# Kernel tuning notes

Measured on AMD Instinct MI355X. Metric: run time of the kernel, lower is better.

The kernel has to match this reference:

```python
import jax, jax.numpy as jnp
import numpy as np
from jax import lax


def setup_inputs() -> dict:
    key = jax.random.key(0)
    ks = jax.random.split(key, 5)
    B, Cin, H, W = 16, 64, 64, 64
    HID, K = 128, 3
    x = jax.random.normal(ks[0], (B, Cin, H, W), jnp.float32)
    w_is = jax.random.normal(ks[1], (4 * HID, Cin, 1, K), jnp.float32) * 0.05
    b_is = jax.random.normal(ks[2], (4 * HID,), jnp.float32) * 0.05
    w_ss = jax.random.normal(ks[3], (4 * HID, HID, 1, K), jnp.float32) * 0.05
    b_ss = jax.random.normal(ks[4], (4 * HID,), jnp.float32) * 0.05
    return {"x": x, "w_is": w_is, "b_is": b_is, "w_ss": w_ss, "b_ss": b_ss}


def reference(x, w_is, b_is, w_ss, b_ss):
    # Shapes: x [B,Cin,H,W]; w_is [4h,Cin,1,k]; w_ss [4h,h,1,k]
    hid = w_ss.shape[1]
    k = w_is.shape[-1]
    pad = k // 2

    # MaskedConv2d mask type 'B' on a (1,k) kernel: keep center and left taps,
    # zero everything strictly right of center.
    mask = (jnp.arange(k) <= pad).astype(x.dtype)  # [k]
    w_is_m = w_is * mask[None, None, None, :]

    # Input-to-state conv over the whole image at once: [B,4h,H,W]
    z_is = lax.conv_general_dilated(
        x, w_is_m, window_strides=(1, 1), padding=[(0, 0), (pad, pad)]
    ) + b_is[None, :, None, None]

    # State-to-state conv is a 1D conv along W: kernel [4h, h, k]
    w1 = w_ss[:, :, 0, :]

    def step(carry, z_row):
        h, c = carry  # each [B, hid, W]
        z = z_row + lax.conv_general_dilated(
            h, w1, window_strides=(1,), padding=[(pad, pad)],
            dimension_numbers=("NCH", "OIH", "NCH"),
        ) + b_ss[None, :, None]
        i_g = jax.nn.sigmoid(z[:, :hid])
        f_g = jax.nn.sigmoid(z[:, hid:2 * hid])
        o_g = jax.nn.sigmoid(z[:, 2 * hid:3 * hid])
        g = jnp.tanh(z[:, 3 * hid:])
        c = f_g * c + i_g * g
        h = o_g * jnp.tanh(c)
        return (h, c), h

    B, _, H, W = x.shape
    h0 = jnp.zeros((B, hid, W), x.dtype)
    c0 = jnp.zeros((B, hid, W), x.dtype)
    zs = jnp.transpose(z_is, (2, 0, 1, 3))  # [H, B, 4h, W]
    _, hs = lax.scan(step, (h0, c0), zs)    # hs: [H, B, hid, W]
    return jnp.transpose(hs, (1, 2, 0, 3))  # [B, hid, H, W]
```

## Files before the change

### kernel.cpp

```cpp
#include <hip/hip_runtime.h>
#include <hip/hip_bf16.h>

#define B_    16
#define CIN   64
#define Hn    64
#define Wn    64
#define HID   128
#define SXS2  72
#define SHS   136
#define NJC   8
#define NBLK  (B_ * NJC)

typedef __attribute__((ext_vector_type(8))) short bfrag_t;
typedef __attribute__((ext_vector_type(4))) float f4_t;

#define HBUF_SHORTS (B_ * Wn * HID)
#define HBUF_BYTES  (HBUF_SHORTS * 2)
#define FLG_STRIDE  256

static __device__ __forceinline__ short f2bf(float f) {
    union { __hip_bfloat16 h; short s; } u;
    u.h = __float2bfloat16(f);
    return u.s;
}
static __device__ __forceinline__ float sigm(float z)  { return 1.f / (1.f + __expf(-z)); }
static __device__ __forceinline__ float tanhf_(float z){ return 2.f / (1.f + __expf(-2.f * z)) - 1.f; }

#define BAR_LGKM() do { \
    asm volatile("s_waitcnt lgkmcnt(0)" ::: "memory"); \
    __builtin_amdgcn_s_barrier(); \
    __builtin_amdgcn_sched_barrier(0); \
} while (0)

#define BAR_VM() do { \
    asm volatile("s_waitcnt vmcnt(0)" ::: "memory"); \
    __builtin_amdgcn_s_barrier(); \
    __builtin_amdgcn_sched_barrier(0); \
} while (0)

extern "C" __global__ __launch_bounds__(256, 1)
void rowlstm_kernel(const float* __restrict__ x,
                    const float* __restrict__ w_is,
                    const float* __restrict__ b_is,
                    const float* __restrict__ w_ss,
                    const float* __restrict__ b_ss,
                    float* __restrict__ out,
                    unsigned char* __restrict__ ws)
{
    const int tid  = threadIdx.x;
    const int bid  = blockIdx.x;
    const int b    = bid & 15;
    const int jc   = bid >> 4;
    const int lane = tid & 63;
    const int wv   = tid >> 6;
    const int l15  = lane & 15;
    const int quad = lane >> 4;

    short*    hbuf0 = (short*)ws;
    unsigned* flags = (unsigned*)(ws + 2 * HBUF_BYTES + b * FLG_STRIDE);

    __shared__ alignas(16) short sH[66 * SHS];
    __shared__ alignas(16) short sX2[65 * SXS2];

    bfrag_t a_frag[4][16];
    #pragma unroll
    for (int mt = 0; mt < 4; ++mt) {
        const int co = mt * HID + jc * 16 + l15;
        #pragma unroll
        for (int kt = 0; kt < 16; ++kt) {
            const int kk0 = kt * 32 + quad * 8;
            const float* p;
            if      (kt < 2)  p = &w_is[(co * CIN + kk0)         * 3 + 0];
            else if (kt < 4)  p = &w_is[(co * CIN + (kk0 - 64))  * 3 + 1];
            else if (kt < 8)  p = &w_ss[(co * HID + (kk0 - 128)) * 3 + 0];
            else if (kt < 12) p = &w_ss[(co * HID + (kk0 - 256)) * 3 + 1];
            else              p = &w_ss[(co * HID + (kk0 - 384)) * 3 + 2];
            bfrag_t v;
            #pragma unroll
            for (int j = 0; j < 8; ++j) v[j] = f2bf(p[j * 3]);
            a_frag[mt][kt] = v;
        }
    }

    float bias[4][4];
    #pragma unroll
    for (int g = 0; g < 4; ++g) {
        #pragma unroll
        for (int r = 0; r < 4; ++r) {
            const int co = g * HID + jc * 16 + quad * 4 + r;
            bias[g][r] = b_is[co] + b_ss[co];
        }
    }

    {
        bfrag_t z8 = {0,0,0,0,0,0,0,0};
        if (tid < 8)  *(bfrag_t*)&sX2[tid * 8] = z8;
        if (tid < 16) {
            *(bfrag_t*)&sH[tid * 8] = z8;
            *(bfrag_t*)&sH[65 * SHS + tid * 8] = z8;
        }
    }

    float creg[4] = {0.f, 0.f, 0.f, 0.f};
    const int wp  = wv * 16 + l15;

    const int xw  = tid & 63;
    const int xc2 = tid >> 6;
    float xr[16];
    #pragma unroll
    for (int e = 0; e < 16; ++e)
        xr[e] = x[((b * CIN + xc2 * 16 + e) * Hn + 0) * Wn + xw];

    const int cig = tid & 15;
    const int w0  = tid >> 4;

    __syncthreads();

    for (int h = 0; h < Hn; ++h) {
        const short* rd_hb = hbuf0 + ((h & 1) ^ 1) * HBUF_SHORTS + b * Wn * HID;
        short*       wr_hb = hbuf0 + (h & 1) * HBUF_SHORTS + b * Wn * HID;

        if (h > 0 && wv == 0) {
            const unsigned tgt = (unsigned)h;
            for (;;) {
                unsigned f = tgt;
                if (lane < NJC)
                    f = __hip_atomic_load(&flags[lane], __ATOMIC_RELAXED, __HIP_MEMORY_SCOPE_AGENT);
                if (__all((int)(f >= tgt))) break;
            }
        }
        BAR_LGKM();

        union { bfrag_t f; unsigned long long q[2]; } hu0, hu1, hu2, hu3;
        if (h > 0) {
            const unsigned long long* s0 = (const unsigned long long*)(rd_hb + (w0     ) * HID + cig * 8);
            const unsigned long long* s1 = (const unsigned long long*)(rd_hb + (w0 + 16) * HID + cig * 8);
            const unsigned long long* s2 = (const unsigned long long*)(rd_hb + (w0 + 32) * HID + cig * 8);
            const unsigned long long* s3 = (const unsigned long long*)(rd_hb + (w0 + 48) * HID + cig * 8);
            hu0.q[0] = __hip_atomic_load(s0,     __ATOMIC_RELAXED, __HIP_MEMORY_SCOPE_AGENT);
            hu0.q[1] = __hip_atomic_load(s0 + 1, __ATOMIC_RELAXED, __HIP_MEMORY_SCOPE_AGENT);
            hu1.q[0] = __hip_atomic_load(s1,     __ATOMIC_RELAXED, __HIP_MEMORY_SCOPE_AGENT);
            hu1.q[1] = __hip_atomic_load(s1 + 1, __ATOMIC_RELAXED, __HIP_MEMORY_SCOPE_AGENT);
            hu2.q[0] = __hip_atomic_load(s2,     __ATOMIC_RELAXED, __HIP_MEMORY_SCOPE_AGENT);
            hu2.q[1] = __hip_atomic_load(s2 + 1, __ATOMIC_RELAXED, __HIP_MEMORY_SCOPE_AGENT);
            hu3.q[0] = __hip_atomic_load(s3,     __ATOMIC_RELAXED, __HIP_MEMORY_SCOPE_AGENT);
            hu3.q[1] = __hip_atomic_load(s3 + 1, __ATOMIC_RELAXED, __HIP_MEMORY_SCOPE_AGENT);
        } else {
            hu0.q[0] = hu0.q[1] = 0ull; hu1.q[0] = hu1.q[1] = 0ull;
            hu2.q[0] = hu2.q[1] = 0ull; hu3.q[0] = hu3.q[1] = 0ull;
        }

        {
            bfrag_t v0, v1;
            #pragma unroll
            for (int e = 0; e < 8; ++e) { v0[e] = f2bf(xr[e]); v1[e] = f2bf(xr[e + 8]); }
            *(bfrag_t*)&sX2[(xw + 1) * SXS2 + xc2 * 16]     = v0;
            *(bfrag_t*)&sX2[(xw + 1) * SXS2 + xc2 * 16 + 8] = v1;
        }
        BAR_LGKM();

        f4_t acc0 = {0.f,0.f,0.f,0.f}, acc1 = {0.f,0.f,0.f,0.f};
        f4_t acc2 = {0.f,0.f,0.f,0.f}, acc3 = {0.f,0.f,0.f,0.f};
        #pragma unroll
        for (int kt = 0; kt < 4; ++kt) {
            const short* src = &sX2[(wp + (kt >> 1)) * SXS2 + (kt & 1) * 32 + quad * 8];
            bfrag_t bf = *(const bfrag_t*)src;
            acc0 = __builtin_amdgcn_mfma_f32_16x16x32_bf16(a_frag[0][kt], bf, acc0, 0, 0, 0);
            acc1 = __builtin_amdgcn_mfma_f32_16x16x32_bf16(a_frag[1][kt], bf, acc1, 0, 0, 0);
            acc2 = __builtin_amdgcn_mfma_f32_16x16x32_bf16(a_frag[2][kt], bf, acc2, 0, 0, 0);
            acc3 = __builtin_amdgcn_mfma_f32_16x16x32_bf16(a_frag[3][kt], bf, acc3, 0, 0, 0);
        }

        *(bfrag_t*)&sH[(w0 +  1) * SHS + cig * 8] = hu0.f;
        *(bfrag_t*)&sH[(w0 + 17) * SHS + cig * 8] = hu1.f;
        *(bfrag_t*)&sH[(w0 + 33) * SHS + cig * 8] = hu2.f;
        *(bfrag_t*)&sH[(w0 + 49) * SHS + cig * 8] = hu3.f;
        BAR_LGKM();

        #pragma unroll
        for (int kt = 4; kt < 16; ++kt) {
            const short* src = &sH[(wp + ((kt - 4) >> 2)) * SHS + ((kt - 4) & 3) * 32 + quad * 8];
            bfrag_t bf = *(const bfrag_t*)src;
            acc0 = __builtin_amdgcn_mfma_f32_16x16x32_bf16(a_frag[0][kt], bf, acc0, 0, 0, 0);
            acc1 = __builtin_amdgcn_mfma_f32_16x16x32_bf16(a_frag[1][kt], bf, acc1, 0, 0, 0);
            acc2 = __builtin_amdgcn_mfma_f32_16x16x32_bf16(a_frag[2][kt], bf, acc2, 0, 0, 0);
            acc3 = __builtin_amdgcn_mfma_f32_16x16x32_bf16(a_frag[3][kt], bf, acc3, 0, 0, 0);
        }

        float hv[4];
        #pragma unroll
        for (int r = 0; r < 4; ++r) {
            float ig = sigm (acc0[r] + bias[0][r]);
            float fg = sigm (acc1[r] + bias[1][r]);
            float og = sigm (acc2[r] + bias[2][r]);
            float gg = tanhf_(acc3[r] + bias[3][r]);
            float c  = fg * creg[r] + ig * gg;
            creg[r]  = c;
            hv[r]    = og * tanhf_(c);
        }

        if (h + 1 < Hn) {
            unsigned p0 = (unsigned)(unsigned short)f2bf(hv[0]) |
                          ((unsigned)(unsigned short)f2bf(hv[1]) << 16);
            unsigned p1 = (unsigned)(unsigned short)f2bf(hv[2]) |
                          ((unsigned)(unsigned short)f2bf(hv[3]) << 16);
            unsigned long long pk = (unsigned long long)p0 | ((unsigned long long)p1 << 32);
            __hip_atomic_store((unsigned long long*)(wr_hb + wp * HID + jc * 16 + quad * 4),
                               pk, __ATOMIC_RELAXED, __HIP_MEMORY_SCOPE_AGENT);
            BAR_VM();
            if (tid == 0)
                __hip_atomic_store(&flags[jc], (unsigned)(h + 1),
                                   __ATOMIC_RELAXED, __HIP_MEMORY_SCOPE_AGENT);
        }

        #pragma unroll
        for (int r = 0; r < 4; ++r)
            out[((b * HID + jc * 16 + quad * 4 + r) * Hn + h) * Wn + wp] = hv[r];

        if (h + 1 < Hn) {
            #pragma unroll
            for (int e = 0; e < 16; ++e)
                xr[e] = x[((b * CIN + xc2 * 16 + e) * Hn + (h + 1)) * Wn + xw];
        }
    }
}

extern "C" void kernel_launch(void* const* d_in, const int* in_sizes, int n_in,
                              void* d_out, int out_size, void* d_ws, size_t ws_size,
                              hipStream_t stream) {
    const float* x    = (const float*)d_in[0];
    const float* w_is = (const float*)d_in[1];
    const float* b_is = (const float*)d_in[2];
    const float* w_ss = (const float*)d_in[3];
    const float* b_ss = (const float*)d_in[4];
    float* out = (float*)d_out;
    unsigned char* ws = (unsigned char*)d_ws;

    hipMemsetAsync(ws + 2 * HBUF_BYTES, 0, B_ * FLG_STRIDE, stream);

    rowlstm_kernel<<<dim3(NBLK), dim3(256), 0, stream>>>(x, w_is, b_is, w_ss, b_ss, out, ws);
}
```

Measured before the change: 321.2 us.

## Load recurrent h directly into MFMA fragments and cut per-step barriers

```diff
diff --git a/kernel.cpp b/kernel.cpp
--- a/kernel.cpp
+++ b/kernel.cpp
@@ -6,10 +6,9 @@
 #define Hn    64
 #define Wn    64
 #define HID   128
-#define SXS2  72
-#define SHS   136
 #define NJC   8
 #define NBLK  (B_ * NJC)
+#define SXROW 160
 
 typedef __attribute__((ext_vector_type(8))) short bfrag_t;
 typedef __attribute__((ext_vector_type(4))) float f4_t;
@@ -28,12 +27,6 @@
 
 #define BAR_LGKM() do { \
     asm volatile("s_waitcnt lgkmcnt(0)" ::: "memory"); \
-    __builtin_amdgcn_s_barrier(); \
-    __builtin_amdgcn_sched_barrier(0); \
-} while (0)
-
-#define BAR_VM() do { \
-    asm volatile("s_waitcnt vmcnt(0)" ::: "memory"); \
     __builtin_amdgcn_s_barrier(); \
     __builtin_amdgcn_sched_barrier(0); \
 } while (0)
@@ -59,8 +52,7 @@
     short*    hbuf0 = (short*)ws;
     unsigned* flags = (unsigned*)(ws + 2 * HBUF_BYTES + b * FLG_STRIDE);
 
-    __shared__ alignas(16) short sH[66 * SHS];
-    __shared__ alignas(16) short sX2[65 * SXS2];
+    __shared__ alignas(16) unsigned char sX2[65 * SXROW];
 
     bfrag_t a_frag[4][16];
     #pragma unroll
@@ -94,11 +86,7 @@
 
     {
         bfrag_t z8 = {0,0,0,0,0,0,0,0};
-        if (tid < 8)  *(bfrag_t*)&sX2[tid * 8] = z8;
-        if (tid < 16) {
-            *(bfrag_t*)&sH[tid * 8] = z8;
-            *(bfrag_t*)&sH[65 * SHS + tid * 8] = z8;
-        }
+        if (tid < 8) *(bfrag_t*)&sX2[tid * 16] = z8;
     }
 
     float creg[4] = {0.f, 0.f, 0.f, 0.f};
@@ -111,80 +99,80 @@
     for (int e = 0; e < 16; ++e)
         xr[e] = x[((b * CIN + xc2 * 16 + e) * Hn + 0) * Wn + xw];
 
-    const int cig = tid & 15;
-    const int w0  = tid >> 4;
-
+    {
+        const int row = xw + 1, sw = (row & 7) << 4;
+        bfrag_t v0, v1;
+        #pragma unroll
+        for (int e = 0; e < 8; ++e) { v0[e] = f2bf(xr[e]); v1[e] = f2bf(xr[e + 8]); }
+        *(bfrag_t*)&sX2[row * SXROW + ((xc2 * 32)      ^ sw)] = v0;
+        *(bfrag_t*)&sX2[row * SXROW + ((xc2 * 32 + 16) ^ sw)] = v1;
+        #pragma unroll
+        for (int e = 0; e < 16; ++e)
+            xr[e] = x[((b * CIN + xc2 * 16 + e) * Hn + 1) * Wn + xw];
+    }
     __syncthreads();
 
     for (int h = 0; h < Hn; ++h) {
         const short* rd_hb = hbuf0 + ((h & 1) ^ 1) * HBUF_SHORTS + b * Wn * HID;
         short*       wr_hb = hbuf0 + (h & 1) * HBUF_SHORTS + b * Wn * HID;
 
-        if (h > 0 && wv == 0) {
+        union { bfrag_t f; unsigned long long q[2]; } bh[12];
+        if (h > 0) {
             const unsigned tgt = (unsigned)h;
             for (;;) {
-                unsigned f = tgt;
-                if (lane < NJC)
-                    f = __hip_atomic_load(&flags[lane], __ATOMIC_RELAXED, __HIP_MEMORY_SCOPE_AGENT);
+                unsigned f = __hip_atomic_load(&flags[lane & 7],
+                                               __ATOMIC_RELAXED, __HIP_MEMORY_SCOPE_AGENT);
                 if (__all((int)(f >= tgt))) break;
-            }
-        }
-        BAR_LGKM();
-
-        union { bfrag_t f; unsigned long long q[2]; } hu0, hu1, hu2, hu3;
-        if (h > 0) {
-            const unsigned long long* s0 = (const unsigned long long*)(rd_hb + (w0     ) * HID + cig * 8);
-            const unsigned long long* s1 = (const unsigned long long*)(rd_hb + (w0 + 16) * HID + cig * 8);
-            const unsigned long long* s2 = (const unsigned long long*)(rd_hb + (w0 + 32) * HID + cig * 8);
-            const unsigned long long* s3 = (const unsigned long long*)(rd_hb + (w0 + 48) * HID + cig * 8);
-            hu0.q[0] = __hip_atomic_load(s0,     __ATOMIC_RELAXED, __HIP_MEMORY_SCOPE_AGENT);
-            hu0.q[1] = __hip_atomic_load(s0 + 1, __ATOMIC_RELAXED, __HIP_MEMORY_SCOPE_AGENT);
-            hu1.q[0] = __hip_atomic_load(s1,     __ATOMIC_RELAXED, __HIP_MEMORY_SCOPE_AGENT);
-            hu1.q[1] = __hip_atomic_load(s1 + 1, __ATOMIC_RELAXED, __HIP_MEMORY_SCOPE_AGENT);
-            hu2.q[0] = __hip_atomic_load(s2,     __ATOMIC_RELAXED, __HIP_MEMORY_SCOPE_AGENT);
-            hu2.q[1] = __hip_atomic_load(s2 + 1, __ATOMIC_RELAXED, __HIP_MEMORY_SCOPE_AGENT);
-            hu3.q[0] = __hip_atomic_load(s3,     __ATOMIC_RELAXED, __HIP_MEMORY_SCOPE_AGENT);
-            hu3.q[1] = __hip_atomic_load(s3 + 1, __ATOMIC_RELAXED, __HIP_MEMORY_SCOPE_AGENT);
-        } else {
-            hu0.q[0] = hu0.q[1] = 0ull; hu1.q[0] = hu1.q[1] = 0ull;
-            hu2.q[0] = hu2.q[1] = 0ull; hu3.q[0] = hu3.q[1] = 0ull;
-        }
-
-        {
-            bfrag_t v0, v1;
-            #pragma unroll
-            for (int e = 0; e < 8; ++e) { v0[e] = f2bf(xr[e]); v1[e] = f2bf(xr[e + 8]); }
-            *(bfrag_t*)&sX2[(xw + 1) * SXS2 + xc2 * 16]     = v0;
-            *(bfrag_t*)&sX2[(xw + 1) * SXS2 + xc2 * 16 + 8] = v1;
-        }
-        BAR_LGKM();
+                __builtin_amdgcn_s_sleep(1);
+            }
+            asm volatile("" ::: "memory");
+
+            #pragma unroll
+            for (int t = 0; t < 3; ++t) {
+                const int  w_read = wp + t - 1;
+                const bool valid  = ((unsigned)w_read < (unsigned)Wn);
+                const short* base = rd_hb + (valid ? w_read : 0) * HID + quad * 8;
+                #pragma unroll
+                for (int cb = 0; cb < 4; ++cb) {
+                    const unsigned long long* s = (const unsigned long long*)(base + cb * 32);
+                    bh[t * 4 + cb].q[0] = __hip_atomic_load(s,     __ATOMIC_RELAXED, __HIP_MEMORY_SCOPE_AGENT);
+                    bh[t * 4 + cb].q[1] = __hip_atomic_load(s + 1, __ATOMIC_RELAXED, __HIP_MEMORY_SCOPE_AGENT);
+                }
+            }
+        }
 
         f4_t acc0 = {0.f,0.f,0.f,0.f}, acc1 = {0.f,0.f,0.f,0.f};
         f4_t acc2 = {0.f,0.f,0.f,0.f}, acc3 = {0.f,0.f,0.f,0.f};
         #pragma unroll
         for (int kt = 0; kt < 4; ++kt) {
-            const short* src = &sX2[(wp + (kt >> 1)) * SXS2 + (kt & 1) * 32 + quad * 8];
-            bfrag_t bf = *(const bfrag_t*)src;
+            const int row  = wp + (kt >> 1);
+            const int boff = ((kt & 1) * 64 + quad * 16) ^ ((row & 7) << 4);
+            bfrag_t bf = *(const bfrag_t*)&sX2[row * SXROW + boff];
             acc0 = __builtin_amdgcn_mfma_f32_16x16x32_bf16(a_frag[0][kt], bf, acc0, 0, 0, 0);
             acc1 = __builtin_amdgcn_mfma_f32_16x16x32_bf16(a_frag[1][kt], bf, acc1, 0, 0, 0);
             acc2 = __builtin_amdgcn_mfma_f32_16x16x32_bf16(a_frag[2][kt], bf, acc2, 0, 0, 0);
             acc3 = __builtin_amdgcn_mfma_f32_16x16x32_bf16(a_frag[3][kt], bf, acc3, 0, 0, 0);
         }
 
-        *(bfrag_t*)&sH[(w0 +  1) * SHS + cig * 8] = hu0.f;
-        *(bfrag_t*)&sH[(w0 + 17) * SHS + cig * 8] = hu1.f;
-        *(bfrag_t*)&sH[(w0 + 33) * SHS + cig * 8] = hu2.f;
-        *(bfrag_t*)&sH[(w0 + 49) * SHS + cig * 8] = hu3.f;
-        BAR_LGKM();
-
-        #pragma unroll
-        for (int kt = 4; kt < 16; ++kt) {
-            const short* src = &sH[(wp + ((kt - 4) >> 2)) * SHS + ((kt - 4) & 3) * 32 + quad * 8];
-            bfrag_t bf = *(const bfrag_t*)src;
-            acc0 = __builtin_amdgcn_mfma_f32_16x16x32_bf16(a_frag[0][kt], bf, acc0, 0, 0, 0);
-            acc1 = __builtin_amdgcn_mfma_f32_16x16x32_bf16(a_frag[1][kt], bf, acc1, 0, 0, 0);
-            acc2 = __builtin_amdgcn_mfma_f32_16x16x32_bf16(a_frag[2][kt], bf, acc2, 0, 0, 0);
-            acc3 = __builtin_amdgcn_mfma_f32_16x16x32_bf16(a_frag[3][kt], bf, acc3, 0, 0, 0);
+        if (h > 0) {
+            asm volatile("s_waitcnt vmcnt(0)" ::: "memory");
+            __builtin_amdgcn_sched_barrier(0);
+            if (wp == 0) {
+                #pragma unroll
+                for (int cb = 0; cb < 4; ++cb) { bh[cb].q[0] = 0ull; bh[cb].q[1] = 0ull; }
+            }
+            if (wp == Wn - 1) {
+                #pragma unroll
+                for (int cb = 0; cb < 4; ++cb) { bh[8 + cb].q[0] = 0ull; bh[8 + cb].q[1] = 0ull; }
+            }
+            #pragma unroll
+            for (int kt = 4; kt < 16; ++kt) {
+                bfrag_t bf = bh[kt - 4].f;
+                acc0 = __builtin_amdgcn_mfma_f32_16x16x32_bf16(a_frag[0][kt], bf, acc0, 0, 0, 0);
+                acc1 = __builtin_amdgcn_mfma_f32_16x16x32_bf16(a_frag[1][kt], bf, acc1, 0, 0, 0);
+                acc2 = __builtin_amdgcn_mfma_f32_16x16x32_bf16(a_frag[2][kt], bf, acc2, 0, 0, 0);
+                acc3 = __builtin_amdgcn_mfma_f32_16x16x32_bf16(a_frag[3][kt], bf, acc3, 0, 0, 0);
+            }
         }
 
         float hv[4];
@@ -207,21 +195,34 @@
             unsigned long long pk = (unsigned long long)p0 | ((unsigned long long)p1 << 32);
             __hip_atomic_store((unsigned long long*)(wr_hb + wp * HID + jc * 16 + quad * 4),
                                pk, __ATOMIC_RELAXED, __HIP_MEMORY_SCOPE_AGENT);
-            BAR_VM();
-            if (tid == 0)
-                __hip_atomic_store(&flags[jc], (unsigned)(h + 1),
-                                   __ATOMIC_RELAXED, __HIP_MEMORY_SCOPE_AGENT);
+        }
+        __syncthreads();
+
+        if (h + 1 < Hn && tid == 0)
+            __hip_atomic_store(&flags[jc], (unsigned)(h + 1),
+                               __ATOMIC_RELAXED, __HIP_MEMORY_SCOPE_AGENT);
+
+        if (h + 1 < Hn) {
+            const int row = xw + 1, sw = (row & 7) << 4;
+            bfrag_t v0, v1;
+            #pragma unroll
+            for (int e = 0; e < 8; ++e) { v0[e] = f2bf(xr[e]); v1[e] = f2bf(xr[e + 8]); }
+            *(bfrag_t*)&sX2[row * SXROW + ((xc2 * 32)      ^ sw)] = v0;
+            *(bfrag_t*)&sX2[row * SXROW + ((xc2 * 32 + 16) ^ sw)] = v1;
         }
 
         #pragma unroll
         for (int r = 0; r < 4; ++r)
             out[((b * HID + jc * 16 + quad * 4 + r) * Hn + h) * Wn + wp] = hv[r];
 
-        if (h + 1 < Hn) {
+        if (h + 2 < Hn) {
             #pragma unroll
             for (int e = 0; e < 16; ++e)
-                xr[e] = x[((b * CIN + xc2 * 16 + e) * Hn + (h + 1)) * Wn + xw];
-        }
+                xr[e] = x[((b * CIN + xc2 * 16 + e) * Hn + (h + 2)) * Wn + xw];
+        }
+
+        if (h + 1 < Hn)
+            BAR_LGKM();
     }
 }
 
```

After: 415.2 us. +29.3%, slower.

## Use per-wave flags with all-lane polling and prestage next x row

Applied to the files above, without the earlier changes.

```diff
diff --git a/kernel.cpp b/kernel.cpp
--- a/kernel.cpp
+++ b/kernel.cpp
@@ -28,12 +28,6 @@
 
 #define BAR_LGKM() do { \
     asm volatile("s_waitcnt lgkmcnt(0)" ::: "memory"); \
-    __builtin_amdgcn_s_barrier(); \
-    __builtin_amdgcn_sched_barrier(0); \
-} while (0)
-
-#define BAR_VM() do { \
-    asm volatile("s_waitcnt vmcnt(0)" ::: "memory"); \
     __builtin_amdgcn_s_barrier(); \
     __builtin_amdgcn_sched_barrier(0); \
 } while (0)
@@ -111,6 +105,17 @@
     for (int e = 0; e < 16; ++e)
         xr[e] = x[((b * CIN + xc2 * 16 + e) * Hn + 0) * Wn + xw];
 
+    {
+        bfrag_t v0, v1;
+        #pragma unroll
+        for (int e = 0; e < 8; ++e) { v0[e] = f2bf(xr[e]); v1[e] = f2bf(xr[e + 8]); }
+        *(bfrag_t*)&sX2[(xw + 1) * SXS2 + xc2 * 16]     = v0;
+        *(bfrag_t*)&sX2[(xw + 1) * SXS2 + xc2 * 16 + 8] = v1;
+        #pragma unroll
+        for (int e = 0; e < 16; ++e)
+            xr[e] = x[((b * CIN + xc2 * 16 + e) * Hn + 1) * Wn + xw];
+    }
+
     const int cig = tid & 15;
     const int w0  = tid >> 4;
 
@@ -120,19 +125,17 @@
         const short* rd_hb = hbuf0 + ((h & 1) ^ 1) * HBUF_SHORTS + b * Wn * HID;
         short*       wr_hb = hbuf0 + (h & 1) * HBUF_SHORTS + b * Wn * HID;
 
-        if (h > 0 && wv == 0) {
+        union { bfrag_t f; unsigned long long q[2]; } hu0, hu1, hu2, hu3;
+        if (h > 0) {
             const unsigned tgt = (unsigned)h;
             for (;;) {
-                unsigned f = tgt;
-                if (lane < NJC)
-                    f = __hip_atomic_load(&flags[lane], __ATOMIC_RELAXED, __HIP_MEMORY_SCOPE_AGENT);
+                unsigned f = __hip_atomic_load(&flags[lane & 31],
+                                               __ATOMIC_RELAXED, __HIP_MEMORY_SCOPE_AGENT);
                 if (__all((int)(f >= tgt))) break;
+                __builtin_amdgcn_s_sleep(1);
             }
-        }
-        BAR_LGKM();
-
-        union { bfrag_t f; unsigned long long q[2]; } hu0, hu1, hu2, hu3;
-        if (h > 0) {
+            asm volatile("" ::: "memory");
+
             const unsigned long long* s0 = (const unsigned long long*)(rd_hb + (w0     ) * HID + cig * 8);
             const unsigned long long* s1 = (const unsigned long long*)(rd_hb + (w0 + 16) * HID + cig * 8);
             const unsigned long long* s2 = (const unsigned long long*)(rd_hb + (w0 + 32) * HID + cig * 8);
@@ -150,15 +153,6 @@
             hu2.q[0] = hu2.q[1] = 0ull; hu3.q[0] = hu3.q[1] = 0ull;
         }
 
-        {
-            bfrag_t v0, v1;
-            #pragma unroll
-            for (int e = 0; e < 8; ++e) { v0[e] = f2bf(xr[e]); v1[e] = f2bf(xr[e + 8]); }
-            *(bfrag_t*)&sX2[(xw + 1) * SXS2 + xc2 * 16]     = v0;
-            *(bfrag_t*)&sX2[(xw + 1) * SXS2 + xc2 * 16 + 8] = v1;
-        }
-        BAR_LGKM();
-
         f4_t acc0 = {0.f,0.f,0.f,0.f}, acc1 = {0.f,0.f,0.f,0.f};
         f4_t acc2 = {0.f,0.f,0.f,0.f}, acc3 = {0.f,0.f,0.f,0.f};
         #pragma unroll
@@ -207,21 +201,34 @@
             unsigned long long pk = (unsigned long long)p0 | ((unsigned long long)p1 << 32);
             __hip_atomic_store((unsigned long long*)(wr_hb + wp * HID + jc * 16 + quad * 4),
                                pk, __ATOMIC_RELAXED, __HIP_MEMORY_SCOPE_AGENT);
-            BAR_VM();
-            if (tid == 0)
-                __hip_atomic_store(&flags[jc], (unsigned)(h + 1),
+            asm volatile("s_waitcnt vmcnt(0)" ::: "memory");
+            if (lane == 0)
+                __hip_atomic_store(&flags[jc * 4 + wv], (unsigned)(h + 1),
                                    __ATOMIC_RELAXED, __HIP_MEMORY_SCOPE_AGENT);
+        }
+
+        __syncthreads();
+
+        if (h + 1 < Hn) {
+            bfrag_t v0, v1;
+            #pragma unroll
+            for (int e = 0; e < 8; ++e) { v0[e] = f2bf(xr[e]); v1[e] = f2bf(xr[e + 8]); }
+            *(bfrag_t*)&sX2[(xw + 1) * SXS2 + xc2 * 16]     = v0;
+            *(bfrag_t*)&sX2[(xw + 1) * SXS2 + xc2 * 16 + 8] = v1;
         }
 
         #pragma unroll
         for (int r = 0; r < 4; ++r)
             out[((b * HID + jc * 16 + quad * 4 + r) * Hn + h) * Wn + wp] = hv[r];
 
-        if (h + 1 < Hn) {
+        if (h + 2 < Hn) {
             #pragma unroll
             for (int e = 0; e < 16; ++e)
-                xr[e] = x[((b * CIN + xc2 * 16 + e) * Hn + (h + 1)) * Wn + xw];
-        }
+                xr[e] = x[((b * CIN + xc2 * 16 + e) * Hn + (h + 2)) * Wn + xw];
+        }
+
+        if (h + 1 < Hn)
+            BAR_LGKM();
     }
 }
 
```

Measured after the change: 314.2 us. -2.2%, faster.
